# Optimization experiments

Measured on AMD Instinct MI355X. Metric: run time of the kernel, lower is better.

The kernel has to match this reference:

```python
import jax, jax.numpy as jnp
import numpy as np

NUM_HEADS = 16

def alibi_slopes(num_heads):
    # 1 / ((2**8)**(1/H))**(i+1) for i in range(H)  -> shape (H, 1, 1)
    x = (2.0 ** 8) ** (1.0 / num_heads)
    return (1.0 / x ** (jnp.arange(1, num_heads + 1, dtype=jnp.float32)))[:, None, None]

def setup_inputs() -> dict:
    key = jax.random.key(0)
    k1, k2, k3 = jax.random.split(key, 3)
    B, T, D = 4, 2048, 1024
    x = jax.random.normal(k1, (B, T, D), dtype=jnp.float32)
    w_qkv = jax.random.normal(k2, (D, 3 * D), dtype=jnp.float32) * 0.02
    w_o = jax.random.normal(k3, (D, D), dtype=jnp.float32) * 0.02
    return {"x": x, "w_qkv": w_qkv, "w_o": w_o}

def reference(x, w_qkv, w_o):
    B, T, C = x.shape
    H = NUM_HEADS
    dh = C // H
    qkv = x @ w_qkv                                   # [B, T, 3C]
    q, k, v = jnp.split(qkv, 3, axis=-1)
    # b t (h d) -> b h t d
    q = q.reshape(B, T, H, dh).transpose(0, 2, 1, 3)
    k = k.reshape(B, T, H, dh).transpose(0, 2, 1, 3)
    v = v.reshape(B, T, H, dh).transpose(0, 2, 1, 3)
    wei = jnp.einsum('bhqd,bhkd->bhqk', q, k)         # [B, H, T, T]
    rel = (jnp.arange(T)[None, :] - jnp.arange(T)[:, None]).astype(jnp.float32)
    bias = alibi_slopes(H) * rel                      # [H, T, T]
    scale = jnp.float32(C) ** 0.5                     # note: full dim C, as in source
    scores = wei / scale + bias
    causal = jnp.tril(jnp.ones((T, T), dtype=bool))
    scores = jnp.where(causal, scores, jnp.float32(-jnp.inf))
    attn = jax.nn.softmax(scores, axis=-1)
    out = jnp.einsum('bhqk,bhkd->bhqd', attn, v)      # [B, H, T, dh]
    concat = out.transpose(0, 2, 1, 3).reshape(B, T, C)
    return concat @ w_o
```

## Files before the change

### kernel.cpp

```cpp
#include <hip/hip_runtime.h>
#include <hip/hip_bf16.h>

typedef float f32x4 __attribute__((ext_vector_type(4)));
typedef short bf16x8 __attribute__((ext_vector_type(8)));
typedef short bf16x4 __attribute__((ext_vector_type(4)));

static __device__ __forceinline__ short f2bs(float f) {
  __hip_bfloat16 h = __float2bfloat16(f);
  union { __hip_bfloat16 h; short s; } u;
  u.h = h;
  return u.s;
}

#define GLDS(gp, lp) __builtin_amdgcn_global_load_lds( \
    (const __attribute__((address_space(1))) unsigned int*)(gp), \
    (__attribute__((address_space(3))) unsigned int*)(lp), 16, 0, 0)

__global__ __launch_bounds__(256) void prep(const float* __restrict__ x,
                                            const float* __restrict__ w_qkv,
                                            const float* __restrict__ w_o,
                                            short* __restrict__ xb,
                                            short* __restrict__ wqkvT,
                                            short* __restrict__ woT) {
  __shared__ float tile[32][33];
  const int bid = blockIdx.x;
  if (bid < 8192) {
    int i = bid * 256 + threadIdx.x;
    f32x4 v = ((const f32x4*)x)[i];
    bf16x4 o;
    o[0] = f2bs(v[0]); o[1] = f2bs(v[1]); o[2] = f2bs(v[2]); o[3] = f2bs(v[3]);
    ((bf16x4*)xb)[i] = o;
    return;
  }
  const float* in; short* out; int R, C, bx, by;
  if (bid < 11264) {
    int b2 = bid - 8192;
    in = w_qkv; out = wqkvT; R = 1024; C = 3072;
    bx = (b2 % 96) * 32; by = (b2 / 96) * 32;
  } else {
    int b3 = bid - 11264;
    in = w_o; out = woT; R = 1024; C = 1024;
    bx = (b3 % 32) * 32; by = (b3 / 32) * 32;
  }
  const int tx = threadIdx.x & 31;
  const int ty = threadIdx.x >> 5;
#pragma unroll
  for (int i = 0; i < 32; i += 8)
    tile[ty + i][tx] = in[(long)(by + ty + i) * C + bx + tx];
  __syncthreads();
#pragma unroll
  for (int i = 0; i < 32; i += 8)
    out[(long)(bx + ty + i) * R + by + tx] = f2bs(tile[tx][ty + i]);
}

__device__ __forceinline__ void gemm_compute_tile(const short* Ac, const short* Bc,
                                                  int r0, int c0, int lr, int quad,
                                                  f32x4 acc[4][4]) {
  const int rq = (quad ^ ((lr >> 1) & 3)) * 8;
  bf16x8 af[4], bfr[4];
#pragma unroll
  for (int i = 0; i < 4; ++i)
    af[i] = *(const bf16x8*)(Ac + (r0 + i * 16 + lr) * 32 + rq);
#pragma unroll
  for (int j = 0; j < 4; ++j)
    bfr[j] = *(const bf16x8*)(Bc + (c0 + j * 16 + lr) * 32 + rq);
#pragma unroll
  for (int i = 0; i < 4; ++i)
#pragma unroll
    for (int j = 0; j < 4; ++j)
      acc[i][j] = __builtin_amdgcn_mfma_f32_16x16x32_bf16(af[i], bfr[j], acc[i][j], 0, 0, 0);
}

__device__ __forceinline__ void gemm_mainloop(const short* __restrict__ A,
                                              const short* __restrict__ Bt,
                                              int K, int rowA0, int rowB0,
                                              short* As, short* Bs,
                                              f32x4 acc[4][4]) {
  const int tid = threadIdx.x;
  const int wave = tid >> 6;
  const int lane = tid & 63;
  const int lr = lane & 15;
  const int quad = lane >> 4;
  const int swz = ((lane & 3) ^ ((lane >> 3) & 3)) * 8;
  const short* aP = A + (long)(rowA0 + wave * 32 + (lane >> 2)) * K + swz;
  const short* bP = Bt + (long)(rowB0 + wave * 32 + (lane >> 2)) * K + swz;
  const int woff = wave * 32 * 32;
  const int r0 = (wave >> 1) * 64;
  const int c0 = (wave & 1) * 64;
  const int c16K = 16 * K;
  const int BUF = 128 * 32;
  GLDS(aP, As + woff);
  GLDS(aP + c16K, As + woff + 16 * 32);
  GLDS(bP, Bs + woff);
  GLDS(bP + c16K, Bs + woff + 16 * 32);
  aP += 32; bP += 32;
  const int nIter = K >> 5;
#pragma unroll 1
  for (int i = 0; i < nIter; i += 2) {
    __syncthreads();
    if (i + 1 < nIter) {
      GLDS(aP, As + BUF + woff);
      GLDS(aP + c16K, As + BUF + woff + 16 * 32);
      GLDS(bP, Bs + BUF + woff);
      GLDS(bP + c16K, Bs + BUF + woff + 16 * 32);
      aP += 32; bP += 32;
    }
    gemm_compute_tile(As, Bs, r0, c0, lr, quad, acc);
    __syncthreads();
    if (i + 2 < nIter) {
      GLDS(aP, As + woff);
      GLDS(aP + c16K, As + woff + 16 * 32);
      GLDS(bP, Bs + woff);
      GLDS(bP + c16K, Bs + woff + 16 * 32);
      aP += 32; bP += 32;
    }
    gemm_compute_tile(As + BUF, Bs + BUF, r0, c0, lr, quad, acc);
  }
}

__global__ __launch_bounds__(256, 5) void gemm_qkv(const short* __restrict__ xb,
                                                   const short* __restrict__ wT,
                                                   short* __restrict__ q,
                                                   short* __restrict__ k,
                                                   short* __restrict__ vt) {
  __shared__ __align__(16) short As[2 * 128 * 32];
  __shared__ __align__(16) short Bs[2 * 128 * 32];
  f32x4 acc[4][4];
#pragma unroll
  for (int i = 0; i < 4; ++i)
#pragma unroll
    for (int j = 0; j < 4; ++j)
      acc[i][j] = (f32x4){0.f, 0.f, 0.f, 0.f};
  const int tileM = blockIdx.x * 128;
  const int tileN = blockIdx.y * 128;
  gemm_mainloop(xb, wT, 1024, tileM, tileN, As, Bs, acc);
  const int tid = threadIdx.x;
  const int wave = tid >> 6;
  const int lane = tid & 63;
  const int lr = lane & 15;
  const int quad = lane >> 4;
  const int wrow = wave >> 1;
  const int wcol = wave & 1;
#pragma unroll
  for (int i = 0; i < 4; ++i) {
    const int row0 = tileM + wrow * 64 + i * 16 + quad * 4;
    const int b = row0 >> 11;
    const int t = row0 & 2047;
#pragma unroll
    for (int j = 0; j < 4; ++j) {
      int col = tileN + wcol * 64 + j * 16 + lr;
      int region = col >> 10;
      int w = col & 1023;
      int h = w >> 6;
      int d = w & 63;
      long bh = (long)b * 16 + h;
      if (region == 0) {
#pragma unroll
        for (int r = 0; r < 4; ++r)
          q[(bh * 2048 + t + r) * 64 + d] = f2bs(acc[i][j][r] * 0.03125f);
      } else if (region == 1) {
#pragma unroll
        for (int r = 0; r < 4; ++r)
          k[(bh * 2048 + t + r) * 64 + d] = f2bs(acc[i][j][r]);
      } else {
        bf16x4 pk;
#pragma unroll
        for (int r = 0; r < 4; ++r) pk[r] = f2bs(acc[i][j][r]);
        *(bf16x4*)(vt + (bh * 64 + d) * 2048 + t) = pk;
      }
    }
  }
}

__global__ __launch_bounds__(256, 5) void attn(const short* __restrict__ q,
                                               const short* __restrict__ kk,
                                               const short* __restrict__ vt,
                                               short* __restrict__ cat) {
  __shared__ __align__(16) short Ks[64 * 72];
  __shared__ __align__(16) short Vs[64 * 72];
  __shared__ __align__(16) short Ps[4 * 16 * 72];
  const int bx = blockIdx.x;
  const int g = bx >> 8;
  const int hshift = ((g & 1) << 3) | ((g & 2) << 1) | ((g & 4) >> 1);
  const int j = 31 - (bx >> 6);
  const int bh = (bx + hshift) & 63;
  const int h = bh & 15;
  const int b = bh >> 4;
  const int tid = threadIdx.x;
  const int wave = tid >> 6;
  const int lane = tid & 63;
  const int lr = lane & 15;
  const int quad = lane >> 4;
  const float l2e = 1.44269504f;
  const float slope = exp2f(-0.5f * (float)(h + 1));
  const float slope_l2e = slope * l2e;
  const float c2 = -2.0f * l2e;
  const int d_cut = (int)ceilf(20.0f * exp2f(0.5f * (float)(h + 1)));
  const short* kbg = kk + (long)bh * 2048 * 64;
  const short* vbg = vt + (long)bh * 64 * 2048;
  const int srow = tid >> 3;
  const int scol = (tid & 7) * 8;
  short* pw = Ps + wave * 16 * 72;

  const int q0 = j * 64;
  const int mrow0 = q0 + wave * 16;
  const int kt_start = max(0, (q0 - d_cut) >> 6);
  const short* qptr = q + ((long)bh * 2048 + mrow0) * 64;
  bf16x8 qf0 = *(const bf16x8*)(qptr + (long)lr * 64 + quad * 8);
  bf16x8 qf1 = *(const bf16x8*)(qptr + (long)lr * 64 + 32 + quad * 8);
  float lp = 0.f;
  f32x4 O[4];
#pragma unroll
  for (int dt = 0; dt < 4; ++dt) O[dt] = (f32x4){0.f, 0.f, 0.f, 0.f};
  float bias[4][4];
  unsigned okbits = 0;
#pragma unroll
  for (int ct = 0; ct < 4; ++ct)
#pragma unroll
    for (int r = 0; r < 4; ++r) {
      int off = ct * 16 + quad * 4 + r;
      bias[ct][r] = slope_l2e * (float)(kt_start * 64 + off - mrow0 - lr) + c2;
      if (off - wave * 16 - lr <= 0) okbits |= 1u << (ct * 4 + r);
    }
  const float bstep = slope_l2e * 64.0f;

  const short* kg = kbg + (long)kt_start * 64 * 64;
  const short* vg = vbg + kt_start * 64;
  bf16x8 pk0 = *(const bf16x8*)(kg + srow * 64 + scol);
  bf16x8 pk1 = *(const bf16x8*)(kg + (srow + 32) * 64 + scol);
  bf16x8 pv0 = *(const bf16x8*)(vg + (long)srow * 2048 + scol);
  bf16x8 pv1 = *(const bf16x8*)(vg + (long)(srow + 32) * 2048 + scol);
  for (int kt = kt_start; kt <= j; ++kt) {
    *(bf16x8*)(Ks + srow * 72 + scol) = pk0;
    *(bf16x8*)(Ks + (srow + 32) * 72 + scol) = pk1;
    *(bf16x8*)(Vs + srow * 72 + scol) = pv0;
    *(bf16x8*)(Vs + (srow + 32) * 72 + scol) = pv1;
    __syncthreads();
    if (kt < j) {
      const short* kg2 = kbg + (long)(kt + 1) * 64 * 64;
      const short* vg2 = vbg + (kt + 1) * 64;
      pk0 = *(const bf16x8*)(kg2 + srow * 64 + scol);
      pk1 = *(const bf16x8*)(kg2 + (srow + 32) * 64 + scol);
      pv0 = *(const bf16x8*)(vg2 + (long)srow * 2048 + scol);
      pv1 = *(const bf16x8*)(vg2 + (long)(srow + 32) * 2048 + scol);
    }
    f32x4 S[4];
    __builtin_amdgcn_s_setprio(1);
#pragma unroll
    for (int ct = 0; ct < 4; ++ct) {
      bf16x8 kf0 = *(const bf16x8*)(Ks + (ct * 16 + lr) * 72 + quad * 8);
      bf16x8 kf1 = *(const bf16x8*)(Ks + (ct * 16 + lr) * 72 + 32 + quad * 8);
      f32x4 a = (f32x4){0.f, 0.f, 0.f, 0.f};
      a = __builtin_amdgcn_mfma_f32_16x16x32_bf16(kf0, qf0, a, 0, 0, 0);
      a = __builtin_amdgcn_mfma_f32_16x16x32_bf16(kf1, qf1, a, 0, 0, 0);
      S[ct] = a;
    }
    __builtin_amdgcn_s_setprio(0);
    const bool diag = (kt == j);
#pragma unroll
    for (int ct = 0; ct < 4; ++ct) {
      bf16x4 pkt;
#pragma unroll
      for (int r = 0; r < 4; ++r) {
        float arg = fmaf(S[ct][r], l2e, bias[ct][r]);
        if (diag && !(okbits & (1u << (ct * 4 + r)))) arg = -10000.0f;
        float p = exp2f(arg);
        lp += p;
        pkt[r] = f2bs(p);
        bias[ct][r] += bstep;
      }
      *(bf16x4*)(pw + lr * 72 + ct * 16 + quad * 4) = pkt;
    }
    asm volatile("s_waitcnt lgkmcnt(0)" ::: "memory");
    bf16x8 pf0 = *(const bf16x8*)(pw + lr * 72 + quad * 8);
    bf16x8 pf1 = *(const bf16x8*)(pw + lr * 72 + 32 + quad * 8);
    __builtin_amdgcn_s_setprio(1);
#pragma unroll
    for (int dt = 0; dt < 4; ++dt) {
      bf16x8 vf0 = *(const bf16x8*)(Vs + (dt * 16 + lr) * 72 + quad * 8);
      bf16x8 vf1 = *(const bf16x8*)(Vs + (dt * 16 + lr) * 72 + 32 + quad * 8);
      O[dt] = __builtin_amdgcn_mfma_f32_16x16x32_bf16(pf0, vf0, O[dt], 0, 0, 0);
      O[dt] = __builtin_amdgcn_mfma_f32_16x16x32_bf16(pf1, vf1, O[dt], 0, 0, 0);
    }
    __builtin_amdgcn_s_setprio(0);
    __syncthreads();
  }
  lp += __shfl_xor(lp, 16);
  lp += __shfl_xor(lp, 32);
#pragma unroll
  for (int r = 0; r < 4; ++r) {
    float lm = __shfl(lp, quad * 4 + r);
    float inv = 1.0f / lm;
    int t = mrow0 + quad * 4 + r;
#pragma unroll
    for (int dt = 0; dt < 4; ++dt)
      cat[((long)b * 2048 + t) * 1024 + h * 64 + dt * 16 + lr] =
          f2bs(O[dt][r] * inv);
  }
}

__global__ __launch_bounds__(256, 5) void gemm_out(const short* __restrict__ cat,
                                                   const short* __restrict__ woT,
                                                   float* __restrict__ out) {
  __shared__ __align__(16) short As[2 * 128 * 32];
  __shared__ __align__(16) short Bs[2 * 128 * 32];
  f32x4 acc[4][4];
#pragma unroll
  for (int i = 0; i < 4; ++i)
#pragma unroll
    for (int j = 0; j < 4; ++j)
      acc[i][j] = (f32x4){0.f, 0.f, 0.f, 0.f};
  const int tileM = blockIdx.x * 128;
  const int tileN = blockIdx.y * 128;
  gemm_mainloop(cat, woT, 1024, tileM, tileN, As, Bs, acc);
  const int tid = threadIdx.x;
  const int wave = tid >> 6;
  const int lane = tid & 63;
  const int lr = lane & 15;
  const int quad = lane >> 4;
#pragma unroll
  for (int i = 0; i < 4; ++i)
#pragma unroll
    for (int j = 0; j < 4; ++j) {
      int col = tileN + (wave & 1) * 64 + j * 16 + lr;
#pragma unroll
      for (int r = 0; r < 4; ++r) {
        int row = tileM + (wave >> 1) * 64 + i * 16 + quad * 4 + r;
        out[(long)row * 1024 + col] = acc[i][j][r];
      }
    }
}

extern "C" void kernel_launch(void* const* d_in, const int* in_sizes, int n_in,
                              void* d_out, int out_size, void* d_ws, size_t ws_size,
                              hipStream_t stream) {
  const float* x = (const float*)d_in[0];
  const float* w_qkv = (const float*)d_in[1];
  const float* w_o = (const float*)d_in[2];
  float* out = (float*)d_out;
  short* ws = (short*)d_ws;
  short* xb = ws;
  short* wqkvT = xb + 8388608;
  short* woT = wqkvT + 3145728;
  short* q = woT + 1048576;
  short* kb = q + 8388608;
  short* vt = kb + 8388608;

  prep<<<12288, 256, 0, stream>>>(x, w_qkv, w_o, xb, wqkvT, woT);
  gemm_qkv<<<dim3(64, 24), 256, 0, stream>>>(xb, wqkvT, q, kb, vt);
  attn<<<dim3(2048), 256, 0, stream>>>(q, kb, vt, xb );
  gemm_out<<<dim3(64, 8), 256, 0, stream>>>(xb, woT, out);
}
```

Baseline: 247.2 us.

## Rewrite QKV GEMM with 256x256 tiles, 8 waves and ping-pong pipelined staging

The QKV projection GEMM moves from 128x128 tiles with 4 waves to 256x256 tiles with 8 waves, using 128KB of LDS double-buffered at K=64 per stage. Global-to-LDS loads for the next stage are split into four chunks, each interleaved with a quarter of the MFMA work and separated by barriers, with raised priority during MFMA bursts. The larger tile raises arithmetic intensity and cuts redundant global/L2 traffic. In exchange it adds many barriers, heavy register use (128 accumulator floats per lane), low occupancy, and a grid of only 384 blocks, which may underfill the GPU.

```diff
diff --git a/kernel.cpp b/kernel.cpp
--- a/kernel.cpp
+++ b/kernel.cpp
@@ -15,6 +15,9 @@
 #define GLDS(gp, lp) __builtin_amdgcn_global_load_lds( \
     (const __attribute__((address_space(1))) unsigned int*)(gp), \
     (__attribute__((address_space(3))) unsigned int*)(lp), 16, 0, 0)
+
+#define MFMA16(a, b, c) __builtin_amdgcn_mfma_f32_16x16x32_bf16((a), (b), (c), 0, 0, 0)
+#define FENCE asm volatile("" ::: "memory")
 
 __global__ __launch_bounds__(256) void prep(const float* __restrict__ x,
                                             const float* __restrict__ w_qkv,
@@ -68,7 +71,7 @@
   for (int i = 0; i < 4; ++i)
 #pragma unroll
     for (int j = 0; j < 4; ++j)
-      acc[i][j] = __builtin_amdgcn_mfma_f32_16x16x32_bf16(af[i], bfr[j], acc[i][j], 0, 0, 0);
+      acc[i][j] = MFMA16(af[i], bfr[j], acc[i][j]);
 }
 
 __device__ __forceinline__ void gemm_mainloop(const short* __restrict__ A,
@@ -118,54 +121,188 @@
   }
 }
 
-__global__ __launch_bounds__(256, 5) void gemm_qkv(const short* __restrict__ xb,
+__global__ __launch_bounds__(512, 2) void gemm_qkv(const short* __restrict__ xb,
                                                    const short* __restrict__ wT,
                                                    short* __restrict__ q,
                                                    short* __restrict__ k,
                                                    short* __restrict__ vt) {
-  __shared__ __align__(16) short As[2 * 128 * 32];
-  __shared__ __align__(16) short Bs[2 * 128 * 32];
-  f32x4 acc[4][4];
-#pragma unroll
-  for (int i = 0; i < 4; ++i)
+  __shared__ __align__(16) char L[131072];
+  const int K = 1024;
+  const int NT = 16;
+  const int tileM = blockIdx.x * 256;
+  const int tileN = blockIdx.y * 256;
+  const int tid = threadIdx.x;
+  const int w = tid >> 6, l = tid & 63;
+  const int lr = l & 15, quad = l >> 4;
+  const int wr = w >> 2, wc = w & 3;
+  const int sr = l >> 3;
+  const int scb = (l & 7) ^ sr;
+  const short* aS = xb + (long)(tileM + w * 16 + sr) * K + scb * 8;
+  const short* bS = wT + (long)(tileN + w * 16 + sr) * K + scb * 8;
+  const int aD = w * 2048 + l * 16;
+  const int bD = 32768 + w * 2048 + l * 16;
+  const int swz0 = (quad ^ (lr & 7)) * 16;
+  const int swz1 = ((4 + quad) ^ (lr & 7)) * 16;
+  const int aR = wr * 16384 + lr * 128;
+  const int bR = 32768 + (wc >> 1) * 16384 + ((wc & 1) * 64 + lr) * 128;
+  const long h128K = (long)128 * K;
+
+  f32x4 acc[8][4];
+#pragma unroll
+  for (int i = 0; i < 8; ++i)
 #pragma unroll
     for (int j = 0; j < 4; ++j)
       acc[i][j] = (f32x4){0.f, 0.f, 0.f, 0.f};
-  const int tileM = blockIdx.x * 128;
-  const int tileN = blockIdx.y * 128;
-  gemm_mainloop(xb, wT, 1024, tileM, tileN, As, Bs, acc);
-  const int tid = threadIdx.x;
-  const int wave = tid >> 6;
-  const int lane = tid & 63;
-  const int lr = lane & 15;
-  const int quad = lane >> 4;
-  const int wrow = wave >> 1;
-  const int wcol = wave & 1;
-#pragma unroll
-  for (int i = 0; i < 4; ++i) {
-    const int row0 = tileM + wrow * 64 + i * 16 + quad * 4;
+  bf16x8 aF[4][2], bF[2][2];
+
+#define STG(src, dst) GLDS((src), (short*)(L + (dst)))
+#pragma unroll
+  for (int h = 0; h < 2; ++h) {
+    STG(aS + h * h128K,         h * 16384 + aD);
+    STG(aS + h * h128K + 8 * K, h * 16384 + aD + 1024);
+    STG(bS + h * h128K,         h * 16384 + bD);
+    STG(bS + h * h128K + 8 * K, h * 16384 + bD + 1024);
+  }
+
+#pragma unroll 1
+  for (int kt = 0; kt < NT; ++kt) {
+    const int db = (kt & 1) << 16;
+    const int sb = db ^ 65536;
+    const bool nxt = (kt + 1 < NT);
+    const long kOff = (long)(kt + 1) * 64;
+    if (nxt) {
+      STG(aS + kOff,         sb + aD);
+      STG(aS + 8 * K + kOff, sb + aD + 1024);
+      asm volatile("s_waitcnt vmcnt(2)" ::: "memory");
+    } else {
+      asm volatile("s_waitcnt vmcnt(0)" ::: "memory");
+    }
+    __builtin_amdgcn_s_barrier();
+    FENCE;
+#pragma unroll
+    for (int mi = 0; mi < 4; ++mi) {
+      aF[mi][0] = *(const bf16x8*)(L + db + aR + mi * 2048 + swz0);
+      aF[mi][1] = *(const bf16x8*)(L + db + aR + mi * 2048 + swz1);
+    }
+#pragma unroll
+    for (int ni = 0; ni < 2; ++ni) {
+      bF[ni][0] = *(const bf16x8*)(L + db + bR + ni * 2048 + swz0);
+      bF[ni][1] = *(const bf16x8*)(L + db + bR + ni * 2048 + swz1);
+    }
+    if (nxt) {
+      STG(aS + h128K + kOff,               sb + 16384 + aD);
+      STG(aS + h128K + 8 * K + kOff,       sb + 16384 + aD + 1024);
+    }
+    FENCE;
+    __builtin_amdgcn_s_barrier();
+    FENCE;
+    __builtin_amdgcn_s_setprio(1);
+#pragma unroll
+    for (int mi = 0; mi < 4; ++mi)
+#pragma unroll
+      for (int ni = 0; ni < 2; ++ni) {
+        acc[mi][ni] = MFMA16(aF[mi][0], bF[ni][0], acc[mi][ni]);
+        acc[mi][ni] = MFMA16(aF[mi][1], bF[ni][1], acc[mi][ni]);
+      }
+    __builtin_amdgcn_s_setprio(0);
+    FENCE;
+    __builtin_amdgcn_s_barrier();
+    FENCE;
+#pragma unroll
+    for (int ni = 0; ni < 2; ++ni) {
+      bF[ni][0] = *(const bf16x8*)(L + db + bR + (2 + ni) * 2048 + swz0);
+      bF[ni][1] = *(const bf16x8*)(L + db + bR + (2 + ni) * 2048 + swz1);
+    }
+    if (nxt) {
+      STG(bS + kOff,         sb + bD);
+      STG(bS + 8 * K + kOff, sb + bD + 1024);
+    }
+    FENCE;
+    __builtin_amdgcn_s_barrier();
+    FENCE;
+    __builtin_amdgcn_s_setprio(1);
+#pragma unroll
+    for (int mi = 0; mi < 4; ++mi)
+#pragma unroll
+      for (int ni = 0; ni < 2; ++ni) {
+        acc[mi][2 + ni] = MFMA16(aF[mi][0], bF[ni][0], acc[mi][2 + ni]);
+        acc[mi][2 + ni] = MFMA16(aF[mi][1], bF[ni][1], acc[mi][2 + ni]);
+      }
+    __builtin_amdgcn_s_setprio(0);
+    FENCE;
+    __builtin_amdgcn_s_barrier();
+    FENCE;
+#pragma unroll
+    for (int mi = 0; mi < 4; ++mi) {
+      aF[mi][0] = *(const bf16x8*)(L + db + aR + (4 + mi) * 2048 + swz0);
+      aF[mi][1] = *(const bf16x8*)(L + db + aR + (4 + mi) * 2048 + swz1);
+    }
+    if (nxt) {
+      STG(bS + h128K + kOff,         sb + 16384 + bD);
+      STG(bS + h128K + 8 * K + kOff, sb + 16384 + bD + 1024);
+    }
+    FENCE;
+    __builtin_amdgcn_s_barrier();
+    FENCE;
+    __builtin_amdgcn_s_setprio(1);
+#pragma unroll
+    for (int mi = 0; mi < 4; ++mi)
+#pragma unroll
+      for (int ni = 0; ni < 2; ++ni) {
+        acc[4 + mi][2 + ni] = MFMA16(aF[mi][0], bF[ni][0], acc[4 + mi][2 + ni]);
+        acc[4 + mi][2 + ni] = MFMA16(aF[mi][1], bF[ni][1], acc[4 + mi][2 + ni]);
+      }
+    __builtin_amdgcn_s_setprio(0);
+    FENCE;
+    __builtin_amdgcn_s_barrier();
+    FENCE;
+#pragma unroll
+    for (int ni = 0; ni < 2; ++ni) {
+      bF[ni][0] = *(const bf16x8*)(L + db + bR + ni * 2048 + swz0);
+      bF[ni][1] = *(const bf16x8*)(L + db + bR + ni * 2048 + swz1);
+    }
+    FENCE;
+    __builtin_amdgcn_s_barrier();
+    FENCE;
+    __builtin_amdgcn_s_setprio(1);
+#pragma unroll
+    for (int mi = 0; mi < 4; ++mi)
+#pragma unroll
+      for (int ni = 0; ni < 2; ++ni) {
+        acc[4 + mi][ni] = MFMA16(aF[mi][0], bF[ni][0], acc[4 + mi][ni]);
+        acc[4 + mi][ni] = MFMA16(aF[mi][1], bF[ni][1], acc[4 + mi][ni]);
+      }
+    __builtin_amdgcn_s_setprio(0);
+    FENCE;
+    __builtin_amdgcn_s_barrier();
+    FENCE;
+  }
+#undef STG
+#pragma unroll
+  for (int mt = 0; mt < 8; ++mt) {
+    const int row0 = tileM + wr * 128 + mt * 16 + quad * 4;
     const int b = row0 >> 11;
     const int t = row0 & 2047;
 #pragma unroll
-    for (int j = 0; j < 4; ++j) {
-      int col = tileN + wcol * 64 + j * 16 + lr;
+    for (int nt = 0; nt < 4; ++nt) {
+      int col = tileN + wc * 64 + nt * 16 + lr;
       int region = col >> 10;
-      int w = col & 1023;
-      int h = w >> 6;
-      int d = w & 63;
+      int ww = col & 1023;
+      int h = ww >> 6;
+      int d = ww & 63;
       long bh = (long)b * 16 + h;
       if (region == 0) {
 #pragma unroll
         for (int r = 0; r < 4; ++r)
-          q[(bh * 2048 + t + r) * 64 + d] = f2bs(acc[i][j][r] * 0.03125f);
+          q[(bh * 2048 + t + r) * 64 + d] = f2bs(acc[mt][nt][r] * 0.03125f);
       } else if (region == 1) {
 #pragma unroll
         for (int r = 0; r < 4; ++r)
-          k[(bh * 2048 + t + r) * 64 + d] = f2bs(acc[i][j][r]);
+          k[(bh * 2048 + t + r) * 64 + d] = f2bs(acc[mt][nt][r]);
       } else {
         bf16x4 pk;
 #pragma unroll
-        for (int r = 0; r < 4; ++r) pk[r] = f2bs(acc[i][j][r]);
+        for (int r = 0; r < 4; ++r) pk[r] = f2bs(acc[mt][nt][r]);
         *(bf16x4*)(vt + (bh * 64 + d) * 2048 + t) = pk;
       }
     }
@@ -251,8 +388,8 @@
       bf16x8 kf0 = *(const bf16x8*)(Ks + (ct * 16 + lr) * 72 + quad * 8);
       bf16x8 kf1 = *(const bf16x8*)(Ks + (ct * 16 + lr) * 72 + 32 + quad * 8);
       f32x4 a = (f32x4){0.f, 0.f, 0.f, 0.f};
-      a = __builtin_amdgcn_mfma_f32_16x16x32_bf16(kf0, qf0, a, 0, 0, 0);
-      a = __builtin_amdgcn_mfma_f32_16x16x32_bf16(kf1, qf1, a, 0, 0, 0);
+      a = MFMA16(kf0, qf0, a);
+      a = MFMA16(kf1, qf1, a);
       S[ct] = a;
     }
     __builtin_amdgcn_s_setprio(0);
@@ -279,8 +416,8 @@
     for (int dt = 0; dt < 4; ++dt) {
       bf16x8 vf0 = *(const bf16x8*)(Vs + (dt * 16 + lr) * 72 + quad * 8);
       bf16x8 vf1 = *(const bf16x8*)(Vs + (dt * 16 + lr) * 72 + 32 + quad * 8);
-      O[dt] = __builtin_amdgcn_mfma_f32_16x16x32_bf16(pf0, vf0, O[dt], 0, 0, 0);
-      O[dt] = __builtin_amdgcn_mfma_f32_16x16x32_bf16(pf1, vf1, O[dt], 0, 0, 0);
+      O[dt] = MFMA16(pf0, vf0, O[dt]);
+      O[dt] = MFMA16(pf1, vf1, O[dt]);
     }
     __builtin_amdgcn_s_setprio(0);
     __syncthreads();
@@ -347,7 +484,7 @@
   short* vt = kb + 8388608;
 
   prep<<<12288, 256, 0, stream>>>(x, w_qkv, w_o, xb, wqkvT, woT);
-  gemm_qkv<<<dim3(64, 24), 256, 0, stream>>>(xb, wqkvT, q, kb, vt);
+  gemm_qkv<<<dim3(32, 12), 512, 0, stream>>>(xb, wqkvT, q, kb, vt);
   attn<<<dim3(2048), 256, 0, stream>>>(q, kb, vt, xb );
   gemm_out<<<dim3(64, 8), 256, 0, stream>>>(xb, woT, out);
 }
```

Result: no change. 244.2 us (-1.2%).

## Load K/V fragments directly from global memory in attention, drop LDS staging

Applied to the files above, without the earlier changes.

The attention kernel no longer stages K and V tiles through shared memory with register prefetch and block barriers. Each wave now reads its MFMA K and V fragments straight from global memory, relying on L1/L2 caching, since every wave reads the same tiles. This removes two __syncthreads per iteration and frees LDS, and occupancy is raised to 6 blocks per CU. The cost is four times redundant global/L1 traffic per block and no software prefetch, so load latency is exposed on the MFMA critical path.

```diff
diff --git a/kernel.cpp b/kernel.cpp
--- a/kernel.cpp
+++ b/kernel.cpp
@@ -15,6 +15,8 @@
 #define GLDS(gp, lp) __builtin_amdgcn_global_load_lds( \
     (const __attribute__((address_space(1))) unsigned int*)(gp), \
     (__attribute__((address_space(3))) unsigned int*)(lp), 16, 0, 0)
+
+#define MFMA16(a, b, c) __builtin_amdgcn_mfma_f32_16x16x32_bf16((a), (b), (c), 0, 0, 0)
 
 __global__ __launch_bounds__(256) void prep(const float* __restrict__ x,
                                             const float* __restrict__ w_qkv,
@@ -68,7 +70,7 @@
   for (int i = 0; i < 4; ++i)
 #pragma unroll
     for (int j = 0; j < 4; ++j)
-      acc[i][j] = __builtin_amdgcn_mfma_f32_16x16x32_bf16(af[i], bfr[j], acc[i][j], 0, 0, 0);
+      acc[i][j] = MFMA16(af[i], bfr[j], acc[i][j]);
 }
 
 __device__ __forceinline__ void gemm_mainloop(const short* __restrict__ A,
@@ -172,12 +174,10 @@
   }
 }
 
-__global__ __launch_bounds__(256, 5) void attn(const short* __restrict__ q,
+__global__ __launch_bounds__(256, 6) void attn(const short* __restrict__ q,
                                                const short* __restrict__ kk,
                                                const short* __restrict__ vt,
                                                short* __restrict__ cat) {
-  __shared__ __align__(16) short Ks[64 * 72];
-  __shared__ __align__(16) short Vs[64 * 72];
   __shared__ __align__(16) short Ps[4 * 16 * 72];
   const int bx = blockIdx.x;
   const int g = bx >> 8;
@@ -198,8 +198,6 @@
   const int d_cut = (int)ceilf(20.0f * exp2f(0.5f * (float)(h + 1)));
   const short* kbg = kk + (long)bh * 2048 * 64;
   const short* vbg = vt + (long)bh * 64 * 2048;
-  const int srow = tid >> 3;
-  const int scol = (tid & 7) * 8;
   short* pw = Ps + wave * 16 * 72;
 
   const int q0 = j * 64;
@@ -224,35 +222,19 @@
     }
   const float bstep = slope_l2e * 64.0f;
 
-  const short* kg = kbg + (long)kt_start * 64 * 64;
-  const short* vg = vbg + kt_start * 64;
-  bf16x8 pk0 = *(const bf16x8*)(kg + srow * 64 + scol);
-  bf16x8 pk1 = *(const bf16x8*)(kg + (srow + 32) * 64 + scol);
-  bf16x8 pv0 = *(const bf16x8*)(vg + (long)srow * 2048 + scol);
-  bf16x8 pv1 = *(const bf16x8*)(vg + (long)(srow + 32) * 2048 + scol);
+  const short* kg = kbg + ((long)kt_start * 64 + lr) * 64 + quad * 8;
+  const short* vg = vbg + (long)lr * 2048 + kt_start * 64 + quad * 8;
+
   for (int kt = kt_start; kt <= j; ++kt) {
-    *(bf16x8*)(Ks + srow * 72 + scol) = pk0;
-    *(bf16x8*)(Ks + (srow + 32) * 72 + scol) = pk1;
-    *(bf16x8*)(Vs + srow * 72 + scol) = pv0;
-    *(bf16x8*)(Vs + (srow + 32) * 72 + scol) = pv1;
-    __syncthreads();
-    if (kt < j) {
-      const short* kg2 = kbg + (long)(kt + 1) * 64 * 64;
-      const short* vg2 = vbg + (kt + 1) * 64;
-      pk0 = *(const bf16x8*)(kg2 + srow * 64 + scol);
-      pk1 = *(const bf16x8*)(kg2 + (srow + 32) * 64 + scol);
-      pv0 = *(const bf16x8*)(vg2 + (long)srow * 2048 + scol);
-      pv1 = *(const bf16x8*)(vg2 + (long)(srow + 32) * 2048 + scol);
-    }
     f32x4 S[4];
     __builtin_amdgcn_s_setprio(1);
 #pragma unroll
     for (int ct = 0; ct < 4; ++ct) {
-      bf16x8 kf0 = *(const bf16x8*)(Ks + (ct * 16 + lr) * 72 + quad * 8);
-      bf16x8 kf1 = *(const bf16x8*)(Ks + (ct * 16 + lr) * 72 + 32 + quad * 8);
+      bf16x8 kf0 = *(const bf16x8*)(kg + ct * 16 * 64);
+      bf16x8 kf1 = *(const bf16x8*)(kg + ct * 16 * 64 + 32);
       f32x4 a = (f32x4){0.f, 0.f, 0.f, 0.f};
-      a = __builtin_amdgcn_mfma_f32_16x16x32_bf16(kf0, qf0, a, 0, 0, 0);
-      a = __builtin_amdgcn_mfma_f32_16x16x32_bf16(kf1, qf1, a, 0, 0, 0);
+      a = MFMA16(kf0, qf0, a);
+      a = MFMA16(kf1, qf1, a);
       S[ct] = a;
     }
     __builtin_amdgcn_s_setprio(0);
@@ -277,13 +259,14 @@
     __builtin_amdgcn_s_setprio(1);
 #pragma unroll
     for (int dt = 0; dt < 4; ++dt) {
-      bf16x8 vf0 = *(const bf16x8*)(Vs + (dt * 16 + lr) * 72 + quad * 8);
-      bf16x8 vf1 = *(const bf16x8*)(Vs + (dt * 16 + lr) * 72 + 32 + quad * 8);
-      O[dt] = __builtin_amdgcn_mfma_f32_16x16x32_bf16(pf0, vf0, O[dt], 0, 0, 0);
-      O[dt] = __builtin_amdgcn_mfma_f32_16x16x32_bf16(pf1, vf1, O[dt], 0, 0, 0);
+      bf16x8 vf0 = *(const bf16x8*)(vg + dt * 16 * 2048);
+      bf16x8 vf1 = *(const bf16x8*)(vg + dt * 16 * 2048 + 32);
+      O[dt] = MFMA16(pf0, vf0, O[dt]);
+      O[dt] = MFMA16(pf1, vf1, O[dt]);
     }
     __builtin_amdgcn_s_setprio(0);
-    __syncthreads();
+    kg += 64 * 64;
+    vg += 64;
   }
   lp += __shfl_xor(lp, 16);
   lp += __shfl_xor(lp, 32);
```

Result: slower. 336.4 us (+36.1%).

## Keep softmax probabilities in registers and permute V reads to match MFMA layout

Applied to the files above, without the earlier changes.

Removes the per-wave shared-memory round trip for the P tile. The exp'd scores are packed straight into bf16x8 registers, and the reduction dimension of the PV MFMA is permuted to match the S accumulator layout. V is now read with two bf16x4 loads per fragment at matching k offsets, and the LDS row stride changes from 72 to 76. Removing the P buffer shrinks LDS use, so the occupancy hint rises from 5 to 6 blocks. The trade-off is more, narrower LDS reads for V, possible bank conflicts at the new stride, and higher register pressure under the tighter launch bound.

```diff
diff --git a/kernel.cpp b/kernel.cpp
--- a/kernel.cpp
+++ b/kernel.cpp
@@ -15,6 +15,8 @@
 #define GLDS(gp, lp) __builtin_amdgcn_global_load_lds( \
     (const __attribute__((address_space(1))) unsigned int*)(gp), \
     (__attribute__((address_space(3))) unsigned int*)(lp), 16, 0, 0)
+
+#define MFMA16(a, b, c) __builtin_amdgcn_mfma_f32_16x16x32_bf16((a), (b), (c), 0, 0, 0)
 
 __global__ __launch_bounds__(256) void prep(const float* __restrict__ x,
                                             const float* __restrict__ w_qkv,
@@ -68,7 +70,7 @@
   for (int i = 0; i < 4; ++i)
 #pragma unroll
     for (int j = 0; j < 4; ++j)
-      acc[i][j] = __builtin_amdgcn_mfma_f32_16x16x32_bf16(af[i], bfr[j], acc[i][j], 0, 0, 0);
+      acc[i][j] = MFMA16(af[i], bfr[j], acc[i][j]);
 }
 
 __device__ __forceinline__ void gemm_mainloop(const short* __restrict__ A,
@@ -172,13 +174,12 @@
   }
 }
 
-__global__ __launch_bounds__(256, 5) void attn(const short* __restrict__ q,
+__global__ __launch_bounds__(256, 6) void attn(const short* __restrict__ q,
                                                const short* __restrict__ kk,
                                                const short* __restrict__ vt,
                                                short* __restrict__ cat) {
-  __shared__ __align__(16) short Ks[64 * 72];
-  __shared__ __align__(16) short Vs[64 * 72];
-  __shared__ __align__(16) short Ps[4 * 16 * 72];
+  __shared__ __align__(16) short Ks[64 * 76];
+  __shared__ __align__(16) short Vs[64 * 76];
   const int bx = blockIdx.x;
   const int g = bx >> 8;
   const int hshift = ((g & 1) << 3) | ((g & 2) << 1) | ((g & 4) >> 1);
@@ -200,7 +201,6 @@
   const short* vbg = vt + (long)bh * 64 * 2048;
   const int srow = tid >> 3;
   const int scol = (tid & 7) * 8;
-  short* pw = Ps + wave * 16 * 72;
 
   const int q0 = j * 64;
   const int mrow0 = q0 + wave * 16;
@@ -231,10 +231,10 @@
   bf16x8 pv0 = *(const bf16x8*)(vg + (long)srow * 2048 + scol);
   bf16x8 pv1 = *(const bf16x8*)(vg + (long)(srow + 32) * 2048 + scol);
   for (int kt = kt_start; kt <= j; ++kt) {
-    *(bf16x8*)(Ks + srow * 72 + scol) = pk0;
-    *(bf16x8*)(Ks + (srow + 32) * 72 + scol) = pk1;
-    *(bf16x8*)(Vs + srow * 72 + scol) = pv0;
-    *(bf16x8*)(Vs + (srow + 32) * 72 + scol) = pv1;
+    *(bf16x8*)(Ks + srow * 76 + scol) = pk0;
+    *(bf16x8*)(Ks + (srow + 32) * 76 + scol) = pk1;
+    *(bf16x8*)(Vs + srow * 76 + scol) = pv0;
+    *(bf16x8*)(Vs + (srow + 32) * 76 + scol) = pv1;
     __syncthreads();
     if (kt < j) {
       const short* kg2 = kbg + (long)(kt + 1) * 64 * 64;
@@ -248,39 +248,41 @@
     __builtin_amdgcn_s_setprio(1);
 #pragma unroll
     for (int ct = 0; ct < 4; ++ct) {
-      bf16x8 kf0 = *(const bf16x8*)(Ks + (ct * 16 + lr) * 72 + quad * 8);
-      bf16x8 kf1 = *(const bf16x8*)(Ks + (ct * 16 + lr) * 72 + 32 + quad * 8);
+      bf16x8 kf0 = *(const bf16x8*)(Ks + (ct * 16 + lr) * 76 + quad * 8);
+      bf16x8 kf1 = *(const bf16x8*)(Ks + (ct * 16 + lr) * 76 + 32 + quad * 8);
       f32x4 a = (f32x4){0.f, 0.f, 0.f, 0.f};
-      a = __builtin_amdgcn_mfma_f32_16x16x32_bf16(kf0, qf0, a, 0, 0, 0);
-      a = __builtin_amdgcn_mfma_f32_16x16x32_bf16(kf1, qf1, a, 0, 0, 0);
+      a = MFMA16(kf0, qf0, a);
+      a = MFMA16(kf1, qf1, a);
       S[ct] = a;
     }
     __builtin_amdgcn_s_setprio(0);
     const bool diag = (kt == j);
+    bf16x8 p8[2];
 #pragma unroll
     for (int ct = 0; ct < 4; ++ct) {
-      bf16x4 pkt;
 #pragma unroll
       for (int r = 0; r < 4; ++r) {
         float arg = fmaf(S[ct][r], l2e, bias[ct][r]);
         if (diag && !(okbits & (1u << (ct * 4 + r)))) arg = -10000.0f;
         float p = exp2f(arg);
         lp += p;
-        pkt[r] = f2bs(p);
+        p8[ct >> 1][(ct & 1) * 4 + r] = f2bs(p);
         bias[ct][r] += bstep;
       }
-      *(bf16x4*)(pw + lr * 72 + ct * 16 + quad * 4) = pkt;
-    }
-    asm volatile("s_waitcnt lgkmcnt(0)" ::: "memory");
-    bf16x8 pf0 = *(const bf16x8*)(pw + lr * 72 + quad * 8);
-    bf16x8 pf1 = *(const bf16x8*)(pw + lr * 72 + 32 + quad * 8);
+    }
     __builtin_amdgcn_s_setprio(1);
 #pragma unroll
-    for (int dt = 0; dt < 4; ++dt) {
-      bf16x8 vf0 = *(const bf16x8*)(Vs + (dt * 16 + lr) * 72 + quad * 8);
-      bf16x8 vf1 = *(const bf16x8*)(Vs + (dt * 16 + lr) * 72 + 32 + quad * 8);
-      O[dt] = __builtin_amdgcn_mfma_f32_16x16x32_bf16(pf0, vf0, O[dt], 0, 0, 0);
-      O[dt] = __builtin_amdgcn_mfma_f32_16x16x32_bf16(pf1, vf1, O[dt], 0, 0, 0);
+    for (int kk2 = 0; kk2 < 2; ++kk2) {
+#pragma unroll
+      for (int dt = 0; dt < 4; ++dt) {
+        const short* vrow = Vs + (dt * 16 + lr) * 76 + kk2 * 32 + quad * 4;
+        bf16x4 v0 = *(const bf16x4*)(vrow);
+        bf16x4 v1 = *(const bf16x4*)(vrow + 16);
+        bf16x8 vf;
+#pragma unroll
+        for (int e = 0; e < 4; ++e) { vf[e] = v0[e]; vf[4 + e] = v1[e]; }
+        O[dt] = MFMA16(p8[kk2], vf, O[dt]);
+      }
     }
     __builtin_amdgcn_s_setprio(0);
     __syncthreads();
```

Result: slower. 321.4 us (+30.0%).
